# Kernel optimization log

Measured on AMD Instinct MI355X. Metric: run time of the kernel, lower is better.

Reference implementation:

```python
import jax, jax.numpy as jnp
import numpy as np

B, T, VOCAB = 32, 512, 1024
D, H, O, L = 256, 256, 1024, 2


def setup_inputs() -> dict:
    key = jax.random.key(0)
    ks = jax.random.split(key, 7)
    s = 0.02  # keep activations numerically tame across the recurrence
    return {
        "x": jax.random.normal(ks[0], (B, T, VOCAB), dtype=jnp.float32),
        "hidden_states": jax.random.normal(ks[1], (L, H), dtype=jnp.float32),
        "W_emb": jax.random.normal(ks[2], (D, VOCAB), dtype=jnp.float32) * s,
        "W": jax.random.normal(ks[3], (L, H, D), dtype=jnp.float32) * s,
        "U": jax.random.normal(ks[4], (L, H, H), dtype=jnp.float32) * s,
        "V": jax.random.normal(ks[5], (L, D, H), dtype=jnp.float32) * s,
        "W_out": jax.random.normal(ks[6], (O, D), dtype=jnp.float32) * s,
        "stack_length": L,
    }


def reference(x, hidden_states, W_emb, W, U, V, W_out, stack_length):
    # Embedding: Linear(V->D, no bias) => x @ W_emb.T
    inp = jnp.einsum('btv,dv->btd', x, W_emb)  # [B,T,D]
    b = x.shape[0]
    for l in range(stack_length):
        Wl, Ul, Vl = W[l], U[l], V[l]
        h0 = jnp.broadcast_to(hidden_states[l], (b, Ul.shape[0]))  # [B,H]

        def step(h, xt):
            # h_new = W_l x_t + U_l h ; out_t = V_l h_new
            h_new = xt @ Wl.T + h @ Ul.T
            return h_new, h_new @ Vl.T

        _, outs = jax.lax.scan(step, h0, jnp.swapaxes(inp, 0, 1))  # outs: [T,B,D]
        inp = jnp.swapaxes(outs, 0, 1)  # [B,T,D]
    logits = inp @ W_out.T  # [B,T,O]
    # Original applies softmax over dim=1 (the sequence dimension) — keep faithful.
    return jax.nn.softmax(logits, axis=1)
```

## Files before the change

kernel.cpp:

```cpp
#include <hip/hip_runtime.h>
#include <stdint.h>
#include <stddef.h>

typedef short s8v __attribute__((ext_vector_type(8)));
typedef short s4v __attribute__((ext_vector_type(4)));
typedef float f4v __attribute__((ext_vector_type(4)));

#define DEV static __device__ __forceinline__


DEV short f2b(float f) {
  union { float f; uint32_t u; } v; v.f = f;
  uint32_t u = v.u;
  uint32_t r = (u + 0x7fffu + ((u >> 16) & 1u)) >> 16;
  return (short)(uint16_t)r;
}
DEV float b2f(short h) {
  union { uint32_t u; float f; } v; v.u = ((uint32_t)(uint16_t)h) << 16;
  return v.f;
}

DEV void gl_lds16(const void* g, void* l) {
  __builtin_amdgcn_global_load_lds(
      (__attribute__((address_space(1))) void*)(uintptr_t)(g),
      (__attribute__((address_space(3))) void*)(l), 16, 0, 0);
}

DEV int rmap_scan(int m) {
  int b = m >> 9;
  int t = m & 511;
  return ((((b >> 4) << 9) | t) << 4) | (b & 15);
}

DEV int hoff(int s, int k) {
  return ((k >> 5) << 9) + (((k >> 3) & 3) << 7) + (s << 3) + (k & 7);
}

DEV void wgemm_body(const float* __restrict__ Af, const float* __restrict__ Bsrc,
                    short* __restrict__ C, int lda, int ldbs, int ldc,
                    int m0, int n0, int tid, short* As, float* Bf) {
  const int w = tid >> 6, lane = tid & 63, quad = lane >> 4, sid = lane & 15;
  const int wm = (w >> 1) * 64, wn = (w & 1) * 64;

  f4v acc[4][4];
#pragma unroll
  for (int i = 0; i < 4; ++i)
#pragma unroll
    for (int j = 0; j < 4; ++j) acc[i][j] = (f4v){0.f, 0.f, 0.f, 0.f};

  for (int k0 = 0; k0 < 256; k0 += 64) {
#pragma unroll
    for (int q = 0; q < 8; ++q) {
      int lin = q * 256 + tid;
      int kr = lin >> 5, nc = (lin & 31) << 2;
      gl_lds16(Bsrc + (size_t)(k0 + kr) * ldbs + n0 + nc, &Bf[lin << 2]);
    }
#pragma unroll
    for (int q = 0; q < 4; ++q) {
      int lin = q * 256 + tid;
      int row = lin >> 3, kc = (lin & 7) << 3;
      const float* ap = Af + (size_t)(m0 + row) * lda + k0 + kc;
      float4 v0 = *(const float4*)ap;
      float4 v1 = *(const float4*)(ap + 4);
      s8v p;
      p[0] = f2b(v0.x); p[1] = f2b(v0.y); p[2] = f2b(v0.z); p[3] = f2b(v0.w);
      p[4] = f2b(v1.x); p[5] = f2b(v1.y); p[6] = f2b(v1.z); p[7] = f2b(v1.w);
      *(s8v*)&As[row * 72 + kc] = p;
    }
    __syncthreads();
#pragma unroll
    for (int kb = 0; kb < 2; ++kb) {
      s8v af[4], bf[4];
#pragma unroll
      for (int mt = 0; mt < 4; ++mt)
        af[mt] = *(const s8v*)&As[(wm + 16 * mt + sid) * 72 + kb * 32 + quad * 8];
#pragma unroll
      for (int nt = 0; nt < 4; ++nt) {
        s8v b;
#pragma unroll
        for (int j = 0; j < 8; ++j)
          b[j] = f2b(Bf[(kb * 32 + quad * 8 + j) * 128 + wn + 16 * nt + sid]);
        bf[nt] = b;
      }
#pragma unroll
      for (int mt = 0; mt < 4; ++mt)
#pragma unroll
        for (int nt = 0; nt < 4; ++nt)
          acc[mt][nt] = __builtin_amdgcn_mfma_f32_16x16x32_bf16(af[mt], bf[nt], acc[mt][nt], 0, 0, 0);
    }
    __syncthreads();
  }
#pragma unroll
  for (int mt = 0; mt < 4; ++mt)
#pragma unroll
    for (int r = 0; r < 4; ++r) {
      int gm = m0 + wm + 16 * mt + 4 * quad + r;
      size_t ro = (size_t)gm * ldc;
#pragma unroll
      for (int nt = 0; nt < 4; ++nt)
        C[ro + n0 + wn + 16 * nt + sid] = f2b(acc[mt][nt][r]);
    }
}

__global__ __launch_bounds__(256) void wgemm(const float* __restrict__ wemb,
                                             const float* __restrict__ wf,
                                             const float* __restrict__ vfp,
                                             const float* __restrict__ wout,
                                             const float* __restrict__ ufp,
                                             short* __restrict__ a0,
                                             short* __restrict__ a1,
                                             short* __restrict__ a2,
                                             short* __restrict__ ub) {
  __shared__ __align__(16) short As[128 * 72];
  __shared__ __align__(16) float Bf[64 * 128];
  const int blk = blockIdx.x, tid = threadIdx.x;
  if (blk < 16) {
    wgemm_body(wf, wemb, a0, 256, 1024, 1024,
               (blk >> 3) * 128, (blk & 7) * 128, tid, As, Bf);
  } else if (blk < 20) {
    int b = blk - 16;
    wgemm_body(wf + 65536, vfp, a1, 256, 256, 256,
               (b >> 1) * 128, (b & 1) * 128, tid, As, Bf);
  } else if (blk < 36) {
    int b = blk - 20;
    wgemm_body(wout, vfp + 65536, a2, 256, 256, 256,
               (b >> 1) * 128, (b & 1) * 128, tid, As, Bf);
  } else {
    int b = blk - 36;
    const float* src = ufp + (size_t)b * 32768;
    short* dst = ub + (size_t)b * 32768;
#pragma unroll 4
    for (int i = tid; i < 8192; i += 256) {
      float4 v = ((const float4*)src)[i];
      s4v q; q.x = f2b(v.x); q.y = f2b(v.y); q.z = f2b(v.z); q.w = f2b(v.w);
      ((s4v*)dst)[i] = q;
    }
  }
}

__global__ __launch_bounds__(256, 2) void gemm_x(const float* __restrict__ Xf,
                                                 const short* __restrict__ Bw,
                                                 short* __restrict__ C) {
  __shared__ __align__(16) short As[32 * 72];
  __shared__ __align__(16) short Bs[256 * 64];
  const int tid = threadIdx.x;
  const int w = tid >> 6, lane = tid & 63, quad = lane >> 4, sid = lane & 15;
  const int m0 = blockIdx.x * 32;
  const int wn = w * 64;

  f4v acc[2][4];
#pragma unroll
  for (int i = 0; i < 2; ++i)
#pragma unroll
    for (int j = 0; j < 4; ++j) acc[i][j] = (f4v){0.f, 0.f, 0.f, 0.f};

  for (int k0 = 0; k0 < 1024; k0 += 64) {
#pragma unroll
    for (int q = 0; q < 8; ++q) {
      int lin = q * 256 + tid;
      gl_lds16(Bw + (size_t)(lin >> 3) * 1024 + k0 + ((lin & 7) << 3), &Bs[lin << 3]);
    }
    {
      int row = tid >> 3, kc = (tid & 7) << 3;
      const float* ap = &Xf[(size_t)(m0 + row) * 1024 + k0 + kc];
      float4 v0 = *(const float4*)ap;
      float4 v1 = *(const float4*)(ap + 4);
      s8v p;
      p[0] = f2b(v0.x); p[1] = f2b(v0.y); p[2] = f2b(v0.z); p[3] = f2b(v0.w);
      p[4] = f2b(v1.x); p[5] = f2b(v1.y); p[6] = f2b(v1.z); p[7] = f2b(v1.w);
      *(s8v*)&As[row * 72 + kc] = p;
    }
    __syncthreads();
#pragma unroll
    for (int kb = 0; kb < 2; ++kb) {
      s8v af[2], bf[4];
#pragma unroll
      for (int mt = 0; mt < 2; ++mt)
        af[mt] = *(const s8v*)&As[(16 * mt + sid) * 72 + kb * 32 + quad * 8];
#pragma unroll
      for (int nt = 0; nt < 4; ++nt)
        bf[nt] = *(const s8v*)&Bs[(wn + 16 * nt + sid) * 64 + kb * 32 + quad * 8];
#pragma unroll
      for (int mt = 0; mt < 2; ++mt)
#pragma unroll
        for (int nt = 0; nt < 4; ++nt)
          acc[mt][nt] = __builtin_amdgcn_mfma_f32_16x16x32_bf16(af[mt], bf[nt], acc[mt][nt], 0, 0, 0);
    }
    __syncthreads();
  }

#pragma unroll
  for (int mt = 0; mt < 2; ++mt)
#pragma unroll
    for (int r = 0; r < 4; ++r) {
      int gm = m0 + 16 * mt + 4 * quad + r;
      size_t ro = (size_t)rmap_scan(gm) * 256;
#pragma unroll
      for (int nt = 0; nt < 4; ++nt)
        C[ro + wn + 16 * nt + sid] = f2b(acc[mt][nt][r]);
    }
}

__global__ __launch_bounds__(256, 1) void scan_fuse(const short* __restrict__ Ub,
                                                    const short* __restrict__ A1b,
                                                    const short* __restrict__ XcIn,
                                                    short* __restrict__ XcOut,
                                                    const float* __restrict__ hinit) {
  constexpr int CL = 4, WU = 12, NC = 128;
  __shared__ __align__(16) short hT[2][4096];
  const int tid = threadIdx.x;
  const int w = tid >> 6, lane = tid & 63, quad = lane >> 4, sid = lane & 15;
  const int c = blockIdx.x & (NC - 1);
  const int g = blockIdx.x >> 7;

  s8v uf[4][8], vf[4][8];
#pragma unroll
  for (int mt = 0; mt < 4; ++mt)
#pragma unroll
    for (int kb = 0; kb < 8; ++kb) {
      int i = 64 * w + 16 * mt + sid;
      int k = 32 * kb + quad * 8;
      uf[mt][kb] = *(const s8v*)&Ub[i * 256 + k];
      vf[mt][kb] = *(const s8v*)&A1b[i * 256 + k];
    }

  const int t0 = (c * CL <= WU) ? 0 : c * CL - WU;
  const int t1 = (c + 1) * CL;

  for (int idx = tid; idx < 4096; idx += 256) {
    int s = idx >> 8, i = idx & 255;
    hT[0][hoff(s, i)] = (t0 == 0) ? f2b(hinit[i]) : (short)0;
  }
  __syncthreads();

  s4v xcn[4];
  {
    const int xb = (((g << 9) + t0) * 16 + sid) * 256;
#pragma unroll
    for (int mt = 0; mt < 4; ++mt)
      xcn[mt] = *(const s4v*)&XcIn[xb + 64 * w + 16 * mt + 4 * quad];
  }

  int pr = 0;
  for (int t = t0; t <= t1; ++t) {
    s8v bf[8];
#pragma unroll
    for (int kb = 0; kb < 8; ++kb)
      bf[kb] = *(const s8v*)&hT[pr][kb * 512 + quad * 128 + sid * 8];
    const bool doh = (t < t1);
    s4v xcc[4];
    if (doh) {
#pragma unroll
      for (int mt = 0; mt < 4; ++mt) xcc[mt] = xcn[mt];
    }
    if (t + 1 < t1) {
      const int xb = (((g << 9) + (t + 1)) * 16 + sid) * 256;
#pragma unroll
      for (int mt = 0; mt < 4; ++mt)
        xcn[mt] = *(const s4v*)&XcIn[xb + 64 * w + 16 * mt + 4 * quad];
    }

    if (t > c * CL) {
      f4v ax[4];
#pragma unroll
      for (int mt = 0; mt < 4; ++mt) ax[mt] = (f4v){0.f, 0.f, 0.f, 0.f};
#pragma unroll
      for (int kb = 0; kb < 8; ++kb)
#pragma unroll
        for (int mt = 0; mt < 4; ++mt)
          ax[mt] = __builtin_amdgcn_mfma_f32_16x16x32_bf16(vf[mt][kb], bf[kb], ax[mt], 0, 0, 0);
      const int obase = (((g << 9) + (t - 1)) * 16 + sid) * 256;
#pragma unroll
      for (int mt = 0; mt < 4; ++mt) {
        s4v p; p.x = f2b(ax[mt].x); p.y = f2b(ax[mt].y);
        p.z = f2b(ax[mt].z); p.w = f2b(ax[mt].w);
        *(s4v*)&XcOut[obase + 64 * w + 16 * mt + 4 * quad] = p;
      }
    }

    if (doh) {
      f4v acc[4];
#pragma unroll
      for (int mt = 0; mt < 4; ++mt) acc[mt] = (f4v){0.f, 0.f, 0.f, 0.f};
#pragma unroll
      for (int kb = 0; kb < 8; ++kb)
#pragma unroll
        for (int mt = 0; mt < 4; ++mt)
          acc[mt] = __builtin_amdgcn_mfma_f32_16x16x32_bf16(uf[mt][kb], bf[kb], acc[mt], 0, 0, 0);
#pragma unroll
      for (int mt = 0; mt < 4; ++mt) {
        int k0 = 64 * w + 16 * mt + 4 * quad;
        f4v v = acc[mt];
        v.x += b2f(xcc[mt].x); v.y += b2f(xcc[mt].y);
        v.z += b2f(xcc[mt].z); v.w += b2f(xcc[mt].w);
        s4v p; p.x = f2b(v.x); p.y = f2b(v.y); p.z = f2b(v.z); p.w = f2b(v.w);
        *(s4v*)&hT[pr ^ 1][hoff(sid, k0)] = p;
      }
    }
    pr ^= 1;
    __syncthreads();
  }
}

__global__ __launch_bounds__(256, 2) void scan_rnn(const short* __restrict__ Ub,
                                                   const short* __restrict__ XcT,
                                                   short* __restrict__ hbuf,
                                                   const float* __restrict__ hinit) {
  constexpr int CL = 2, WU = 12, NC = 256;
  __shared__ __align__(16) short hT[2][4096];
  const int tid = threadIdx.x;
  const int w = tid >> 6, lane = tid & 63, quad = lane >> 4, sid = lane & 15;
  const int c = blockIdx.x & (NC - 1);
  const int g = blockIdx.x >> 8;

  s8v uf[4][8];
#pragma unroll
  for (int mt = 0; mt < 4; ++mt)
#pragma unroll
    for (int kb = 0; kb < 8; ++kb) {
      int i = 64 * w + 16 * mt + sid;
      int k = 32 * kb + quad * 8;
      uf[mt][kb] = *(const s8v*)&Ub[i * 256 + k];
    }

  const int t0 = (c * CL <= WU) ? 0 : c * CL - WU;
  const int t1 = (c + 1) * CL;

  for (int idx = tid; idx < 4096; idx += 256) {
    int s = idx >> 8, i = idx & 255;
    hT[0][hoff(s, i)] = (t0 == 0) ? f2b(hinit[i]) : (short)0;
  }
  __syncthreads();

  s4v xcn[4];
  {
    const int xb = (((g << 9) + t0) * 16 + sid) * 256;
#pragma unroll
    for (int mt = 0; mt < 4; ++mt)
      xcn[mt] = *(const s4v*)&XcT[xb + 64 * w + 16 * mt + 4 * quad];
  }

  int pr = 0;
  for (int t = t0; t < t1; ++t) {
    s8v bf[8];
#pragma unroll
    for (int kb = 0; kb < 8; ++kb)
      bf[kb] = *(const s8v*)&hT[pr][kb * 512 + quad * 128 + sid * 8];
    s4v xcc[4];
#pragma unroll
    for (int mt = 0; mt < 4; ++mt) xcc[mt] = xcn[mt];
    if (t + 1 < t1) {
      const int xb = (((g << 9) + (t + 1)) * 16 + sid) * 256;
#pragma unroll
      for (int mt = 0; mt < 4; ++mt)
        xcn[mt] = *(const s4v*)&XcT[xb + 64 * w + 16 * mt + 4 * quad];
    }

    f4v acc[4];
#pragma unroll
    for (int mt = 0; mt < 4; ++mt) acc[mt] = (f4v){0.f, 0.f, 0.f, 0.f};
#pragma unroll
    for (int kb = 0; kb < 8; ++kb)
#pragma unroll
      for (int mt = 0; mt < 4; ++mt)
        acc[mt] = __builtin_amdgcn_mfma_f32_16x16x32_bf16(uf[mt][kb], bf[kb], acc[mt], 0, 0, 0);

    const bool emit = (t >= c * CL);
    const int xbase = (((g << 9) + t) * 16 + sid) * 256;
#pragma unroll
    for (int mt = 0; mt < 4; ++mt) {
      int k0 = 64 * w + 16 * mt + 4 * quad;
      f4v v = acc[mt];
      v.x += b2f(xcc[mt].x); v.y += b2f(xcc[mt].y);
      v.z += b2f(xcc[mt].z); v.w += b2f(xcc[mt].w);
      s4v p; p.x = f2b(v.x); p.y = f2b(v.y); p.z = f2b(v.z); p.w = f2b(v.w);
      *(s4v*)&hT[pr ^ 1][hoff(sid, k0)] = p;
      if (emit) *(s4v*)&hbuf[xbase + k0] = p;
    }
    pr ^= 1;
    __syncthreads();
  }
}

__global__ __launch_bounds__(256, 2) void gemm_logsm(const short* __restrict__ A,
                                                     const short* __restrict__ Bw,
                                                     float* __restrict__ out) {
  __shared__ __align__(16) short As[512 * 40];
  __shared__ __align__(16) short Bs[64 * 32];
  __shared__ float2 red[4][64];
  const int tid = threadIdx.x;
  const int w = tid >> 6, lane = tid & 63, quad = lane >> 4, sid = lane & 15;
  const int b = blockIdx.x & 31, ot = blockIdx.x >> 5;
  const int g = b >> 4, si = b & 15;

  f4v acc[8][4];
#pragma unroll
  for (int i = 0; i < 8; ++i)
#pragma unroll
    for (int j = 0; j < 4; ++j) acc[i][j] = (f4v){0.f, 0.f, 0.f, 0.f};

  for (int k0 = 0; k0 < 256; k0 += 32) {
#pragma unroll
    for (int q = 0; q < 8; ++q) {
      int lin = q * 256 + tid;
      int t = lin >> 2, kch = lin & 3;
      size_t ar = ((size_t)(g * 512 + t) * 16 + si) * 256;
      s8v v = *(const s8v*)(A + ar + k0 + kch * 8);
      *(s8v*)&As[t * 40 + kch * 8] = v;
    }
    {
      int row = tid & 63, kch = tid >> 6;
      s8v v = *(const s8v*)(Bw + (size_t)(ot * 64 + row) * 256 + k0 + kch * 8);
      *(s8v*)&Bs[tid << 3] = v;
    }
    __syncthreads();
    s8v bf[4];
#pragma unroll
    for (int nt = 0; nt < 4; ++nt)
      bf[nt] = *(const s8v*)&Bs[(quad * 64 + 16 * nt + sid) * 8];
#pragma unroll
    for (int mt = 0; mt < 8; ++mt) {
      s8v af = *(const s8v*)&As[(128 * w + 16 * mt + sid) * 40 + quad * 8];
#pragma unroll
      for (int nt = 0; nt < 4; ++nt)
        acc[mt][nt] = __builtin_amdgcn_mfma_f32_16x16x32_bf16(af, bf[nt], acc[mt][nt], 0, 0, 0);
    }
    __syncthreads();
  }

#pragma unroll
  for (int nt = 0; nt < 4; ++nt) {
    float m = -3.0e38f;
#pragma unroll
    for (int mt = 0; mt < 8; ++mt)
#pragma unroll
      for (int r = 0; r < 4; ++r) m = fmaxf(m, acc[mt][nt][r]);
    float sum = 0.f;
#pragma unroll
    for (int mt = 0; mt < 8; ++mt)
#pragma unroll
      for (int r = 0; r < 4; ++r) sum += __expf(acc[mt][nt][r] - m);
#pragma unroll
    for (int d = 16; d < 64; d <<= 1) {
      float om = __shfl_xor(m, d, 64);
      float os = __shfl_xor(sum, d, 64);
      float nm = fmaxf(m, om);
      sum = sum * __expf(m - nm) + os * __expf(om - nm);
      m = nm;
    }
    if (quad == 0) red[w][16 * nt + sid] = (float2){m, sum};
  }
  __syncthreads();
#pragma unroll
  for (int nt = 0; nt < 4; ++nt) {
    float M = -3.0e38f, S = 0.f;
#pragma unroll
    for (int ww = 0; ww < 4; ++ww) {
      float2 r2 = red[ww][16 * nt + sid];
      float nm = fmaxf(M, r2.x);
      S = S * __expf(M - nm) + r2.y * __expf(r2.x - nm);
      M = nm;
    }
    const float inv = 1.0f / S;
    const size_t cbase = (size_t)b * 512 * 1024 + ot * 64 + 16 * nt + sid;
#pragma unroll
    for (int mt = 0; mt < 8; ++mt)
#pragma unroll
      for (int r = 0; r < 4; ++r) {
        int t = 128 * w + 16 * mt + 4 * quad + r;
        out[cbase + (size_t)t * 1024] = __expf(acc[mt][nt][r] - M) * inv;
      }
  }
}

extern "C" void kernel_launch(void* const* d_in, const int* in_sizes, int n_in,
                              void* d_out, int out_size, void* d_ws, size_t ws_size,
                              hipStream_t stream) {
  (void)in_sizes; (void)n_in; (void)out_size; (void)ws_size;
  const float* xf   = (const float*)d_in[0];
  const float* hs   = (const float*)d_in[1];
  const float* wemb = (const float*)d_in[2];
  const float* wf   = (const float*)d_in[3];
  const float* ufp  = (const float*)d_in[4];
  const float* vfp  = (const float*)d_in[5];
  const float* wout = (const float*)d_in[6];

  char* ws = (char*)d_ws;
  short* hbuf = (short*)(ws);
  short* xcT0 = (short*)(ws + 8388608);
  short* xcT1 = (short*)(ws + 16777216);
  short* a0   = (short*)(ws + 25165824);
  short* a1   = (short*)(ws + 25690112);
  short* a2   = (short*)(ws + 25821184);
  short* ub   = (short*)(ws + 26345472);

  wgemm<<<40, 256, 0, stream>>>(wemb, wf, vfp, wout, ufp, a0, a1, a2, ub);

  gemm_x<<<512, 256, 0, stream>>>(xf, a0, xcT0);

  scan_fuse<<<256, 256, 0, stream>>>(ub, a1, xcT0, xcT1, hs);

  scan_rnn<<<512, 256, 0, stream>>>(ub + 65536, xcT1, hbuf, hs + 256);

  gemm_logsm<<<512, 256, 0, stream>>>(hbuf, a2, (float*)d_out);
}
```

Measured before the change: 235.0 us.

## Retile scan intermediate layout and stage GEMM epilogues through LDS for coalesced stores

Changes the layout of the intermediate x-projection buffer so each scan block reads and writes contiguous 16-byte chunks per lane instead of strided rows. gemm_x now maps blocks to (batch group, timestep pair) and transposes its output tile through LDS before writing wide vectors. The softmax GEMM epilogue also stages each warp's probabilities in LDS and writes full float4 rows, replacing scattered scalar stores. The cost is extra LDS traffic and several more barriers in the epilogues.

```diff
diff --git a/kernel.cpp b/kernel.cpp
--- a/kernel.cpp
+++ b/kernel.cpp
@@ -24,12 +24,6 @@
   __builtin_amdgcn_global_load_lds(
       (__attribute__((address_space(1))) void*)(uintptr_t)(g),
       (__attribute__((address_space(3))) void*)(l), 16, 0, 0);
-}
-
-DEV int rmap_scan(int m) {
-  int b = m >> 9;
-  int t = m & 511;
-  return ((((b >> 4) << 9) | t) << 4) | (b & 15);
 }
 
 DEV int hoff(int s, int k) {
@@ -145,7 +139,7 @@
   __shared__ __align__(16) short Bs[256 * 64];
   const int tid = threadIdx.x;
   const int w = tid >> 6, lane = tid & 63, quad = lane >> 4, sid = lane & 15;
-  const int m0 = blockIdx.x * 32;
+  const int g = blockIdx.x >> 8, tp = blockIdx.x & 255;
   const int wn = w * 64;
 
   f4v acc[2][4];
@@ -162,7 +156,8 @@
     }
     {
       int row = tid >> 3, kc = (tid & 7) << 3;
-      const float* ap = &Xf[(size_t)(m0 + row) * 1024 + k0 + kc];
+      int m = (g * 16 + (row & 15)) * 512 + 2 * tp + (row >> 4);
+      const float* ap = &Xf[(size_t)m * 1024 + k0 + kc];
       float4 v0 = *(const float4*)ap;
       float4 v1 = *(const float4*)(ap + 4);
       s8v p;
@@ -189,16 +184,32 @@
     __syncthreads();
   }
 
+  short* Ls = Bs;
 #pragma unroll
   for (int mt = 0; mt < 2; ++mt)
 #pragma unroll
-    for (int r = 0; r < 4; ++r) {
-      int gm = m0 + 16 * mt + 4 * quad + r;
-      size_t ro = (size_t)rmap_scan(gm) * 256;
-#pragma unroll
-      for (int nt = 0; nt < 4; ++nt)
-        C[ro + wn + 16 * nt + sid] = f2b(acc[mt][nt][r]);
-    }
+    for (int nt = 0; nt < 4; ++nt) {
+      int n = wn + 16 * nt + sid;
+#pragma unroll
+      for (int r = 0; r < 4; ++r)
+        Ls[(16 * mt + 4 * quad + r) * 264 + n] = f2b(acc[mt][nt][r]);
+    }
+  __syncthreads();
+  {
+    const size_t obase = (size_t)((g << 9) + 2 * tp) * 4096;
+#pragma unroll
+    for (int h = 0; h < 2; ++h) {
+      int q = h * 256 + tid;
+      int tl = q >> 8, q16 = q & 255;
+      int ch = q16 >> 3, qq = q16 & 7;
+      s4v lo = *(const s4v*)&Ls[(tl * 16 + 2 * qq) * 264 + ch * 4];
+      s4v hi = *(const s4v*)&Ls[(tl * 16 + 2 * qq + 1) * 264 + ch * 4];
+      s8v v;
+      v[0] = lo.x; v[1] = lo.y; v[2] = lo.z; v[3] = lo.w;
+      v[4] = hi.x; v[5] = hi.y; v[6] = hi.z; v[7] = hi.w;
+      *(s8v*)&C[obase + (size_t)tl * 4096 + q16 * 8] = v;
+    }
+  }
 }
 
 __global__ __launch_bounds__(256, 1) void scan_fuse(const short* __restrict__ Ub,
@@ -212,6 +223,7 @@
   const int w = tid >> 6, lane = tid & 63, quad = lane >> 4, sid = lane & 15;
   const int c = blockIdx.x & (NC - 1);
   const int g = blockIdx.x >> 7;
+  const int laneoff = quad * 64 + sid * 4;
 
   s8v uf[4][8], vf[4][8];
 #pragma unroll
@@ -235,10 +247,10 @@
 
   s4v xcn[4];
   {
-    const int xb = (((g << 9) + t0) * 16 + sid) * 256;
+    const size_t xb = (size_t)((g << 9) + t0) * 4096 + 1024 * w + laneoff;
 #pragma unroll
     for (int mt = 0; mt < 4; ++mt)
-      xcn[mt] = *(const s4v*)&XcIn[xb + 64 * w + 16 * mt + 4 * quad];
+      xcn[mt] = *(const s4v*)&XcIn[xb + 256 * mt];
   }
 
   int pr = 0;
@@ -254,10 +266,10 @@
       for (int mt = 0; mt < 4; ++mt) xcc[mt] = xcn[mt];
     }
     if (t + 1 < t1) {
-      const int xb = (((g << 9) + (t + 1)) * 16 + sid) * 256;
+      const size_t xb = (size_t)((g << 9) + t + 1) * 4096 + 1024 * w + laneoff;
 #pragma unroll
       for (int mt = 0; mt < 4; ++mt)
-        xcn[mt] = *(const s4v*)&XcIn[xb + 64 * w + 16 * mt + 4 * quad];
+        xcn[mt] = *(const s4v*)&XcIn[xb + 256 * mt];
     }
 
     if (t > c * CL) {
@@ -269,12 +281,12 @@
 #pragma unroll
         for (int mt = 0; mt < 4; ++mt)
           ax[mt] = __builtin_amdgcn_mfma_f32_16x16x32_bf16(vf[mt][kb], bf[kb], ax[mt], 0, 0, 0);
-      const int obase = (((g << 9) + (t - 1)) * 16 + sid) * 256;
+      const size_t ob = (size_t)((g << 9) + (t - 1)) * 4096 + 1024 * w + laneoff;
 #pragma unroll
       for (int mt = 0; mt < 4; ++mt) {
         s4v p; p.x = f2b(ax[mt].x); p.y = f2b(ax[mt].y);
         p.z = f2b(ax[mt].z); p.w = f2b(ax[mt].w);
-        *(s4v*)&XcOut[obase + 64 * w + 16 * mt + 4 * quad] = p;
+        *(s4v*)&XcOut[ob + 256 * mt] = p;
       }
     }
 
@@ -312,6 +324,7 @@
   const int w = tid >> 6, lane = tid & 63, quad = lane >> 4, sid = lane & 15;
   const int c = blockIdx.x & (NC - 1);
   const int g = blockIdx.x >> 8;
+  const int laneoff = quad * 64 + sid * 4;
 
   s8v uf[4][8];
 #pragma unroll
@@ -334,10 +347,10 @@
 
   s4v xcn[4];
   {
-    const int xb = (((g << 9) + t0) * 16 + sid) * 256;
+    const size_t xb = (size_t)((g << 9) + t0) * 4096 + 1024 * w + laneoff;
 #pragma unroll
     for (int mt = 0; mt < 4; ++mt)
-      xcn[mt] = *(const s4v*)&XcT[xb + 64 * w + 16 * mt + 4 * quad];
+      xcn[mt] = *(const s4v*)&XcT[xb + 256 * mt];
   }
 
   int pr = 0;
@@ -350,10 +363,10 @@
 #pragma unroll
     for (int mt = 0; mt < 4; ++mt) xcc[mt] = xcn[mt];
     if (t + 1 < t1) {
-      const int xb = (((g << 9) + (t + 1)) * 16 + sid) * 256;
+      const size_t xb = (size_t)((g << 9) + t + 1) * 4096 + 1024 * w + laneoff;
 #pragma unroll
       for (int mt = 0; mt < 4; ++mt)
-        xcn[mt] = *(const s4v*)&XcT[xb + 64 * w + 16 * mt + 4 * quad];
+        xcn[mt] = *(const s4v*)&XcT[xb + 256 * mt];
     }
 
     f4v acc[4];
@@ -366,7 +379,7 @@
         acc[mt] = __builtin_amdgcn_mfma_f32_16x16x32_bf16(uf[mt][kb], bf[kb], acc[mt], 0, 0, 0);
 
     const bool emit = (t >= c * CL);
-    const int xbase = (((g << 9) + t) * 16 + sid) * 256;
+    const size_t xbase = ((size_t)((g << 9) + t) * 16 + sid) * 256;
 #pragma unroll
     for (int mt = 0; mt < 4; ++mt) {
       int k0 = 64 * w + 16 * mt + 4 * quad;
@@ -428,6 +441,7 @@
     __syncthreads();
   }
 
+  float Mv[4], Iv[4];
 #pragma unroll
   for (int nt = 0; nt < 4; ++nt) {
     float m = -3.0e38f;
@@ -461,15 +475,36 @@
       S = S * __expf(M - nm) + r2.y * __expf(r2.x - nm);
       M = nm;
     }
-    const float inv = 1.0f / S;
-    const size_t cbase = (size_t)b * 512 * 1024 + ot * 64 + 16 * nt + sid;
-#pragma unroll
-    for (int mt = 0; mt < 8; ++mt)
-#pragma unroll
-      for (int r = 0; r < 4; ++r) {
-        int t = 128 * w + 16 * mt + 4 * quad + r;
-        out[cbase + (size_t)t * 1024] = __expf(acc[mt][nt][r] - M) * inv;
+    Mv[nt] = M;
+    Iv[nt] = 1.0f / S;
+  }
+  __syncthreads();
+
+  float* Ps = (float*)As;
+  const size_t obb = (size_t)b * 524288 + ot * 64;
+#pragma unroll
+  for (int ww = 0; ww < 4; ++ww) {
+    if (w == ww) {
+#pragma unroll
+      for (int mt = 0; mt < 8; ++mt)
+#pragma unroll
+        for (int nt = 0; nt < 4; ++nt)
+#pragma unroll
+          for (int r = 0; r < 4; ++r)
+            Ps[(16 * mt + 4 * quad + r) * 68 + 16 * nt + sid] =
+                __expf(acc[mt][nt][r] - Mv[nt]) * Iv[nt];
+    }
+    __syncthreads();
+    {
+      const int tl = tid >> 4, c4 = tid & 15;
+#pragma unroll
+      for (int s2 = 0; s2 < 8; ++s2) {
+        int row = s2 * 16 + tl;
+        float4 v = *(const float4*)&Ps[row * 68 + c4 * 4];
+        *(float4*)&out[obb + (size_t)(ww * 128 + row) * 1024 + c4 * 4] = v;
       }
+    }
+    __syncthreads();
   }
 }
 
```

Result: faster. 226.2 us (-3.7%).
